# Kernel optimization log

Hardware: AMD Instinct MI355X
Metric: run time of the kernel (lower is better)

## Reference

```python
import jax, jax.numpy as jnp
import numpy as np
from jax import lax

N = 1024
N_I = 64
N_AV = 10
ALPHA = 0.5
RHO = 0.9
GAMMA = 1.0


def _make_params(seed=0):
    rng = np.random.RandomState(seed)
    diluition = 1.0 - N_AV / N
    W = rng.uniform(-1, 1, [N, N])
    W = W * (rng.uniform(0, 1, [N, N]) > diluition)
    eig = np.linalg.eigvals(W)
    W = (RHO * W / np.max(np.absolute(eig))).astype(np.float32)
    # N_i != 1 branch: gaussian input weights scaled by gamma
    W_in = (GAMMA * rng.randn(N_I, N)).astype(np.float32)
    return jnp.asarray(W), jnp.asarray(W_in)


def setup_inputs() -> dict:
    key = jax.random.key(0)
    Input = jax.random.normal(key, (128, N_I, 512), dtype=jnp.float32)
    W, W_in = _make_params()
    return {"Input": Input, "W": W, "W_in": W_in}


def reference(Input, W, W_in):
    # Input: [B, N_i, T] -> X: [B, N, T]
    B = Input.shape[0]
    x0 = jnp.zeros((B, W.shape[0]), dtype=Input.dtype)
    seq = jnp.transpose(Input, (2, 0, 1))  # [T, B, N_i]

    def step(x, s):
        x = (1.0 - ALPHA) * x + ALPHA * jnp.tanh(s @ W_in + x @ W)
        return x, x

    _, X = lax.scan(step, x0, seq)  # [T, B, N]
    return jnp.transpose(X, (1, 2, 0))  # [B, N, T]
```

## Files before the change

kernel.cpp:

```cpp
#include <hip/hip_runtime.h>
#include <hip/hip_fp16.h>
#include <cstdint>
#include <cstddef>

#define BB 128
#define NN 1024
#define NI 64
#define TT 512
#define MAXNNZ 16384
#define NE 28
#define TH 16

#define WS_OFFS   0u
#define WS_IDX    16384u
#define WS_VAL    65536u
#define WS_PERM   131072u
#define WS_IPERM  135168u
#define WS_XSTATE 139264u
#define WS_WINP   663552u
#define WS_EIDX2  925696u
#define WS_CNT16  983040u
#define WS_OFF16  1048576u
#define WS_U      1114112u

__global__ __launch_bounds__(64) void k_count16(const float* __restrict__ W, int* __restrict__ cnt16) {
    int bc = blockIdx.x;
    int s = bc & 15, g = bc >> 4;
    int col = g * 64 + threadIdx.x;
    int c = 0;
    for (int q = 0; q < 64; ++q) {
        int k = s * 64 + q;
        c += (W[(size_t)k * NN + col] != 0.0f) ? 1 : 0;
    }
    cnt16[col * 16 + s] = c;
}

__global__ __launch_bounds__(1024) void k_scan3(const int* __restrict__ cnt16, int* __restrict__ offs,
                                                int* __restrict__ off16) {
    __shared__ int s[NN];
    int tid = threadIdx.x;
    int t = 0;
#pragma unroll
    for (int q = 0; q < 16; ++q) t += cnt16[tid * 16 + q];
    s[tid] = t;
    __syncthreads();
    for (int d = 1; d < NN; d <<= 1) {
        int v = (tid >= d) ? s[tid - d] : 0;
        __syncthreads();
        s[tid] += v;
        __syncthreads();
    }
    int incl = s[tid];
    offs[tid + 1] = (incl < MAXNNZ) ? incl : MAXNNZ;
    if (tid == 0) offs[0] = 0;
    int base = incl - t;
#pragma unroll
    for (int q = 0; q < 16; ++q) {
        off16[tid * 16 + q] = base;
        base += cnt16[tid * 16 + q];
    }
}

__global__ __launch_bounds__(64) void k_fill16(const float* __restrict__ W, const int* __restrict__ off16,
                                               unsigned short* __restrict__ idx, float* __restrict__ val) {
    int bc = blockIdx.x;
    int s = bc & 15, g = bc >> 4;
    int col = g * 64 + threadIdx.x;
    int p = off16[col * 16 + s];
    for (int q = 0; q < 64; ++q) {
        int k = s * 64 + q;
        float w = W[(size_t)k * NN + col];
        if (w != 0.0f) { idx[p] = (unsigned short)k; val[p] = w; ++p; }
    }
}

__global__ __launch_bounds__(1024) void k_rankchoice(const int* __restrict__ offs,
        const unsigned short* __restrict__ gidx, int* __restrict__ perm, int* __restrict__ iperm,
        unsigned short* __restrict__ eidx2) {
    __shared__ int sc[NN];
    __shared__ unsigned short rk[NN][NE];
    __shared__ unsigned short scnt[NN];
    __shared__ unsigned short ctr[448][32];
    int n = threadIdx.x;
    sc[n] = offs[n + 1] - offs[n];
    __syncthreads();
    int myc = sc[n];
    int r = 0;
    for (int m = 0; m < NN; ++m) {
        int cm = sc[m];
        r += (cm > myc || (cm == myc && m < n)) ? 1 : 0;
    }
    perm[r] = n;
    iperm[n] = r;
    __syncthreads();
    {
        int rr = n;
        int c = perm[rr];
        int o0 = offs[c];
        int cn = offs[c + 1] - o0;
        if (cn > NE) cn = NE;
        scnt[rr] = (unsigned short)cn;
        for (int j = 0; j < cn; ++j) rk[rr][j] = (unsigned short)iperm[(int)gidx[o0 + j]];
    }
    __syncthreads();
    int tid = n;
    if (tid < 448) {
        int w = tid / NE, j = tid % NE;
        for (int b = 0; b < 32; ++b) ctr[tid][b] = 0;
        int first_addr = -1;
        for (int l = 0; l < 64; ++l) {
            int rr = 64 * w + l;
            if (j < (int)scnt[rr]) {
                int rv = (int)rk[rr][j];
                int bA = rv & 31;
                int bB = (rv ^ (rv >> 5)) & 31;
                int addr;
                if (ctr[tid][bA] <= ctr[tid][bB]) { addr = rv << 2; ctr[tid][bA]++; }
                else { addr = 4096 + (((rv & ~31) | bB) << 2); ctr[tid][bB]++; }
                eidx2[j * NN + rr] = (unsigned short)addr;
                if (first_addr < 0) first_addr = addr;
            }
        }
        unsigned short pad = (unsigned short)(first_addr < 0 ? 0 : first_addr);
        for (int l = 0; l < 64; ++l) {
            int rr = 64 * w + l;
            if (j >= (int)scnt[rr]) eidx2[j * NN + rr] = pad;
        }
    }
}

__global__ __launch_bounds__(256) void k_permwin(const float* __restrict__ Win, const int* __restrict__ perm,
                                                 float* __restrict__ Winp) {
    int idx = blockIdx.x * 256 + threadIdx.x;
    int i = idx >> 10, r = idx & 1023;
    Winp[idx] = Win[(i << 10) + perm[r]];
}

__global__ __launch_bounds__(256) void k_uproj3(const float* __restrict__ In, const float* __restrict__ Winp,
                                                __half* __restrict__ U, int t0c, int nblk) {
    int b  = blockIdx.x / nblk;
    int tq = blockIdx.x % nblk;
    int t0 = t0c + tq * 32;
    __shared__ float s[32][NI + 1];
    int tid = threadIdx.x;
    {
        int i = tid >> 2, g = tid & 3;
        const float* ip = In + ((size_t)b * NI + i) * TT + t0 + g * 8;
        float4 v0 = *(const float4*)(ip);
        float4 v1 = *(const float4*)(ip + 4);
        s[g * 8 + 0][i] = v0.x; s[g * 8 + 1][i] = v0.y;
        s[g * 8 + 2][i] = v0.z; s[g * 8 + 3][i] = v0.w;
        s[g * 8 + 4][i] = v1.x; s[g * 8 + 5][i] = v1.y;
        s[g * 8 + 6][i] = v1.z; s[g * 8 + 7][i] = v1.w;
    }
    __syncthreads();
    const float4* W4 = (const float4*)Winp;
    uint2* U2 = (uint2*)U;
    for (int th = 0; th < 2; ++th) {
        float4 acc[16];
#pragma unroll
        for (int t = 0; t < 16; ++t) acc[t] = make_float4(0.f, 0.f, 0.f, 0.f);
        for (int i = 0; i < NI; ++i) {
            float4 w = W4[(size_t)i * 256 + tid];
#pragma unroll
            for (int t = 0; t < 16; ++t) {
                float sv = s[th * 16 + t][i];
                acc[t].x = fmaf(w.x, sv, acc[t].x);
                acc[t].y = fmaf(w.y, sv, acc[t].y);
                acc[t].z = fmaf(w.z, sv, acc[t].z);
                acc[t].w = fmaf(w.w, sv, acc[t].w);
            }
        }
#pragma unroll
        for (int t = 0; t < 16; ++t) {
            __half2 h01 = __floats2half2_rn(acc[t].x, acc[t].y);
            __half2 h23 = __floats2half2_rn(acc[t].z, acc[t].w);
            uint2 pk;
            pk.x = *(unsigned int*)&h01;
            pk.y = *(unsigned int*)&h23;
            U2[((size_t)(tq * 32 + th * 16 + t) * BB + b) * 256 + tid] = pk;
        }
    }
}

__device__ __forceinline__ float fast_tanh(float z) {
    float a = fabsf(z) * 2.885390082f;
    a = fminf(a, 60.0f);
    float e = __builtin_amdgcn_exp2f(a);
    float r = 1.0f - __fdividef(2.0f, e + 1.0f);
    return z < 0.0f ? -r : r;
}

#define L28(M) \
  M(0) M(1) M(2) M(3) M(4) M(5) M(6) M(7) M(8) M(9) M(10) M(11) M(12) M(13) \
  M(14) M(15) M(16) M(17) M(18) M(19) M(20) M(21) M(22) M(23) M(24) M(25) M(26) M(27)

#define DW(i)  float w##i; int a##i;
#define IW(i)  { a##i = (int)eidx2[(i) * NN + n]; \
                 w##i = (cnt > i) ? gval[o0 + i] : 0.0f; }

#define PIN_ALL \
  asm volatile("" : "+v"(w0),"+v"(w1),"+v"(w2),"+v"(w3),"+v"(w4),"+v"(w5),"+v"(w6),"+v"(w7)); \
  asm volatile("" : "+v"(w8),"+v"(w9),"+v"(w10),"+v"(w11),"+v"(w12),"+v"(w13),"+v"(w14),"+v"(w15)); \
  asm volatile("" : "+v"(w16),"+v"(w17),"+v"(w18),"+v"(w19),"+v"(w20),"+v"(w21),"+v"(w22),"+v"(w23)); \
  asm volatile("" : "+v"(w24),"+v"(w25),"+v"(w26),"+v"(w27)); \
  asm volatile("" : "+v"(a0),"+v"(a1),"+v"(a2),"+v"(a3),"+v"(a4),"+v"(a5),"+v"(a6),"+v"(a7)); \
  asm volatile("" : "+v"(a8),"+v"(a9),"+v"(a10),"+v"(a11),"+v"(a12),"+v"(a13),"+v"(a14),"+v"(a15)); \
  asm volatile("" : "+v"(a16),"+v"(a17),"+v"(a18),"+v"(a19),"+v"(a20),"+v"(a21),"+v"(a22),"+v"(a23)); \
  asm volatile("" : "+v"(a24),"+v"(a25),"+v"(a26),"+v"(a27));

#define GRP(J, i0, i1, i2, i3) \
  if ((J) < wmax) { \
    float q0 = *(const float*)(xp + a##i0); \
    float q1 = *(const float*)(xp + a##i1); \
    float q2 = *(const float*)(xp + a##i2); \
    float q3 = *(const float*)(xp + a##i3); \
    z0 = fmaf(w##i0, q0, z0); z1 = fmaf(w##i1, q1, z1); \
    z2 = fmaf(w##i2, q2, z2); z3 = fmaf(w##i3, q3, z3); \
  }

#define GATHER_ALL \
  GRP(0, 0,1,2,3)      GRP(4, 4,5,6,7)      GRP(8, 8,9,10,11) \
  GRP(12, 12,13,14,15) GRP(16, 16,17,18,19) GRP(20, 20,21,22,23) \
  GRP(24, 24,25,26,27)

#define STEP(PH, XDST) { \
    float u = unx; \
    int tn = t + 1; tn = (tn < Tc) ? tn : (Tc - 1); \
    unx = (float)Ub[(size_t)tn * ustep]; \
    const char* xp = xb + (PH); \
    float z0 = u, z1 = 0.f, z2 = 0.f, z3 = 0.f; \
    GATHER_ALL \
    x = 0.5f * x + 0.5f * fast_tanh((z0 + z1) + (z2 + z3)); \
    XDST = x; \
    float* wb = (float*)(xb + ((PH) ^ 8192)); \
    wb[n] = x; \
    wb[NN + nB] = x; \
    __syncthreads(); \
    ++t; \
}

__global__ __launch_bounds__(1024, 4)
void k_step(const __half* __restrict__ U,
            const int* __restrict__ offs, const unsigned short* __restrict__ eidx2,
            const float* __restrict__ gval, const int* __restrict__ perm,
            float* __restrict__ out, float* __restrict__ xstate, int t0, int Tc) {
    __shared__ float xbuf[2][2][NN];
    int b = blockIdx.x, n = threadIdx.x;
    int c = perm[n];
    int nB = (n & ~31) | ((n ^ (n >> 5)) & 31);

    int o0 = offs[c];
    int cnt = offs[c + 1] - o0;
    L28(DW)
    L28(IW)
    PIN_ALL

    int wmax = cnt;
#pragma unroll
    for (int d = 1; d < 64; d <<= 1) {
        int o = __shfl_xor(wmax, d);
        wmax = wmax > o ? wmax : o;
    }
    wmax = __builtin_amdgcn_readfirstlane(wmax);

    float x = (t0 == 0) ? 0.0f : xstate[((size_t)b << 10) + n];
    xbuf[0][0][n] = x;
    xbuf[0][1][nB] = x;
    __syncthreads();

    char* xb = (char*)&xbuf[0][0][0];
    const __half* Ub = U + (size_t)b * NN + n;
    const size_t ustep = (size_t)BB * NN;
    float unx = (float)Ub[0];

    for (int tb = 0; tb < Tc; tb += TH) {
        PIN_ALL
        int t = tb;
        float y0, y1, y2, y3, y4, y5, y6, y7, y8, y9, y10, y11, y12, y13, y14, y15;
        STEP(0,    y0)
        STEP(8192, y1)
        STEP(0,    y2)
        STEP(8192, y3)
        STEP(0,    y4)
        STEP(8192, y5)
        STEP(0,    y6)
        STEP(8192, y7)
        STEP(0,    y8)
        STEP(8192, y9)
        STEP(0,    y10)
        STEP(8192, y11)
        STEP(0,    y12)
        STEP(8192, y13)
        STEP(0,    y14)
        STEP(8192, y15)
        float4* op = (float4*)(out + ((size_t)b * NN + c) * TT + (size_t)(t0 + tb));
        op[0] = make_float4(y0,  y1,  y2,  y3);
        op[1] = make_float4(y4,  y5,  y6,  y7);
        op[2] = make_float4(y8,  y9,  y10, y11);
        op[3] = make_float4(y12, y13, y14, y15);
    }
    if (Tc < TT) xstate[((size_t)b << 10) + n] = x;
}

extern "C" void kernel_launch(void* const* d_in, const int* in_sizes, int n_in,
                              void* d_out, int out_size, void* d_ws, size_t ws_size,
                              hipStream_t stream) {
    const float* In  = (const float*)d_in[0];
    const float* W   = (const float*)d_in[1];
    const float* Win = (const float*)d_in[2];
    float* out = (float*)d_out;
    char* ws = (char*)d_ws;
    int* offs           = (int*)(ws + WS_OFFS);
    unsigned short* idx = (unsigned short*)(ws + WS_IDX);
    float* val          = (float*)(ws + WS_VAL);
    int* perm           = (int*)(ws + WS_PERM);
    int* iperm          = (int*)(ws + WS_IPERM);
    float* xstate       = (float*)(ws + WS_XSTATE);
    float* Winp         = (float*)(ws + WS_WINP);
    unsigned short* eidx2 = (unsigned short*)(ws + WS_EIDX2);
    int* cnt16          = (int*)(ws + WS_CNT16);
    int* off16          = (int*)(ws + WS_OFF16);
    __half* U           = (__half*)(ws + WS_U);

    int Tc = 32;
    const int cands[5] = {512, 256, 128, 64, 32};
    for (int i = 0; i < 5; ++i) {
        if ((size_t)WS_U + (size_t)cands[i] * BB * NN * 2 <= ws_size) { Tc = cands[i]; break; }
    }

    k_count16<<<256, 64, 0, stream>>>(W, cnt16);
    k_scan3<<<1, 1024, 0, stream>>>(cnt16, offs, off16);
    k_fill16<<<256, 64, 0, stream>>>(W, off16, idx, val);
    k_rankchoice<<<1, 1024, 0, stream>>>(offs, idx, perm, iperm, eidx2);
    k_permwin<<<256, 256, 0, stream>>>(Win, perm, Winp);

    for (int t0 = 0; t0 < TT; t0 += Tc) {
        int nblk = Tc / 32;
        k_uproj3<<<BB * nblk, 256, 0, stream>>>(In, Winp, U, t0, nblk);
        k_step<<<BB, 1024, 0, stream>>>(U, offs, eidx2, val, perm, out, xstate, t0, Tc);
    }
}
```

Measured before the change: 656.2 us.

## Use fp16 dot2 for input projection and rebalance LDS bank assignment

Measured after the change: 670.3 us. 2.1% more time.

```diff
diff --git a/kernel.cpp b/kernel.cpp
--- a/kernel.cpp
+++ b/kernel.cpp
@@ -17,11 +17,25 @@
 #define WS_PERM   131072u
 #define WS_IPERM  135168u
 #define WS_XSTATE 139264u
-#define WS_WINP   663552u
+#define WS_WINPH2 663552u
 #define WS_EIDX2  925696u
 #define WS_CNT16  983040u
 #define WS_OFF16  1048576u
 #define WS_U      1114112u
+
+typedef _Float16 h2 __attribute__((ext_vector_type(2)));
+union U32H2 { unsigned u; h2 h; };
+
+__device__ __forceinline__ float fdot2f(unsigned a, unsigned b, float c) {
+#if __has_builtin(__builtin_amdgcn_fdot2)
+    U32H2 av, bv; av.u = a; bv.u = b;
+    return __builtin_amdgcn_fdot2(av.h, bv.h, c, false);
+#else
+    __half2 ah = *(__half2*)&a, bh = *(__half2*)&b;
+    return fmaf(__low2float(ah), __low2float(bh),
+                fmaf(__high2float(ah), __high2float(bh), c));
+#endif
+}
 
 __global__ __launch_bounds__(64) void k_count16(const float* __restrict__ W, int* __restrict__ cnt16) {
     int bc = blockIdx.x;
@@ -80,7 +94,7 @@
     __shared__ int sc[NN];
     __shared__ unsigned short rk[NN][NE];
     __shared__ unsigned short scnt[NN];
-    __shared__ unsigned short ctr[448][32];
+    __shared__ unsigned char ctr8[448][32];
     int n = threadIdx.x;
     sc[n] = offs[n + 1] - offs[n];
     __syncthreads();
@@ -106,17 +120,44 @@
     int tid = n;
     if (tid < 448) {
         int w = tid / NE, j = tid % NE;
-        for (int b = 0; b < 32; ++b) ctr[tid][b] = 0;
+        unsigned char* mc = &ctr8[tid][0];
+        for (int b = 0; b < 32; ++b) mc[b] = 0;
+        unsigned long long sel = 0ull;
+        for (int l = 0; l < 64; ++l) {
+            int rr = 64 * w + l;
+            if (j < (int)scnt[rr]) {
+                int rv = (int)rk[rr][j];
+                int bA = rv & 31, bB = (rv ^ (rv >> 5)) & 31;
+                if (mc[bA] <= mc[bB]) mc[bA]++;
+                else { sel |= (1ull << l); mc[bB]++; }
+            }
+        }
+        for (int sweep = 0; sweep < 16; ++sweep) {
+            bool ch = false;
+            for (int l = 0; l < 64; ++l) {
+                int rr = 64 * w + l;
+                if (j < (int)scnt[rr]) {
+                    int rv = (int)rk[rr][j];
+                    int bA = rv & 31, bB = (rv ^ (rv >> 5)) & 31;
+                    int isB = (int)((sel >> l) & 1ull);
+                    int cur = isB ? bB : bA, alt = isB ? bA : bB;
+                    if ((int)mc[cur] > (int)mc[alt] + 1) {
+                        mc[cur]--; mc[alt]++;
+                        sel ^= (1ull << l);
+                        ch = true;
+                    }
+                }
+            }
+            if (!ch) break;
+        }
         int first_addr = -1;
         for (int l = 0; l < 64; ++l) {
             int rr = 64 * w + l;
             if (j < (int)scnt[rr]) {
                 int rv = (int)rk[rr][j];
-                int bA = rv & 31;
                 int bB = (rv ^ (rv >> 5)) & 31;
-                int addr;
-                if (ctr[tid][bA] <= ctr[tid][bB]) { addr = rv << 2; ctr[tid][bA]++; }
-                else { addr = 4096 + (((rv & ~31) | bB) << 2); ctr[tid][bB]++; }
+                int addr = ((sel >> l) & 1ull) ? (4096 + (((rv & ~31) | bB) << 2))
+                                               : (rv << 2);
                 eidx2[j * NN + rr] = (unsigned short)addr;
                 if (first_addr < 0) first_addr = addr;
             }
@@ -129,46 +170,55 @@
     }
 }
 
-__global__ __launch_bounds__(256) void k_permwin(const float* __restrict__ Win, const int* __restrict__ perm,
-                                                 float* __restrict__ Winp) {
+__global__ __launch_bounds__(256) void k_permwin2(const float* __restrict__ Win, const int* __restrict__ perm,
+                                                  unsigned* __restrict__ Winph2) {
     int idx = blockIdx.x * 256 + threadIdx.x;
-    int i = idx >> 10, r = idx & 1023;
-    Winp[idx] = Win[(i << 10) + perm[r]];
-}
-
-__global__ __launch_bounds__(256) void k_uproj3(const float* __restrict__ In, const float* __restrict__ Winp,
+    int i2 = idx >> 10, r = idx & 1023;
+    int c = perm[r];
+    unsigned lo = (unsigned)__half_as_ushort(__float2half(Win[(size_t)(2 * i2) * NN + c]));
+    unsigned hi = (unsigned)__half_as_ushort(__float2half(Win[(size_t)(2 * i2 + 1) * NN + c]));
+    Winph2[idx] = lo | (hi << 16);
+}
+
+__global__ __launch_bounds__(256) void k_uproj4(const float* __restrict__ In, const unsigned* __restrict__ Winph2,
                                                 __half* __restrict__ U, int t0c, int nblk) {
     int b  = blockIdx.x / nblk;
     int tq = blockIdx.x % nblk;
     int t0 = t0c + tq * 32;
-    __shared__ float s[32][NI + 1];
+    __shared__ unsigned s2[32][33];
     int tid = threadIdx.x;
     {
         int i = tid >> 2, g = tid & 3;
         const float* ip = In + ((size_t)b * NI + i) * TT + t0 + g * 8;
         float4 v0 = *(const float4*)(ip);
         float4 v1 = *(const float4*)(ip + 4);
-        s[g * 8 + 0][i] = v0.x; s[g * 8 + 1][i] = v0.y;
-        s[g * 8 + 2][i] = v0.z; s[g * 8 + 3][i] = v0.w;
-        s[g * 8 + 4][i] = v1.x; s[g * 8 + 5][i] = v1.y;
-        s[g * 8 + 6][i] = v1.z; s[g * 8 + 7][i] = v1.w;
-    }
-    __syncthreads();
-    const float4* W4 = (const float4*)Winp;
+        __half* row = (__half*)&s2[i >> 1][0];
+        int h = i & 1;
+        row[2 * (g * 8 + 0) + h] = __float2half(v0.x);
+        row[2 * (g * 8 + 1) + h] = __float2half(v0.y);
+        row[2 * (g * 8 + 2) + h] = __float2half(v0.z);
+        row[2 * (g * 8 + 3) + h] = __float2half(v0.w);
+        row[2 * (g * 8 + 4) + h] = __float2half(v1.x);
+        row[2 * (g * 8 + 5) + h] = __float2half(v1.y);
+        row[2 * (g * 8 + 6) + h] = __float2half(v1.z);
+        row[2 * (g * 8 + 7) + h] = __float2half(v1.w);
+    }
+    __syncthreads();
+    const uint4* W4 = (const uint4*)Winph2;
     uint2* U2 = (uint2*)U;
     for (int th = 0; th < 2; ++th) {
         float4 acc[16];
 #pragma unroll
         for (int t = 0; t < 16; ++t) acc[t] = make_float4(0.f, 0.f, 0.f, 0.f);
-        for (int i = 0; i < NI; ++i) {
-            float4 w = W4[(size_t)i * 256 + tid];
+        for (int i2 = 0; i2 < 32; ++i2) {
+            uint4 w = W4[(size_t)i2 * 256 + tid];
 #pragma unroll
             for (int t = 0; t < 16; ++t) {
-                float sv = s[th * 16 + t][i];
-                acc[t].x = fmaf(w.x, sv, acc[t].x);
-                acc[t].y = fmaf(w.y, sv, acc[t].y);
-                acc[t].z = fmaf(w.z, sv, acc[t].z);
-                acc[t].w = fmaf(w.w, sv, acc[t].w);
+                unsigned sv = s2[i2][th * 16 + t];
+                acc[t].x = fdot2f(w.x, sv, acc[t].x);
+                acc[t].y = fdot2f(w.y, sv, acc[t].y);
+                acc[t].z = fdot2f(w.z, sv, acc[t].z);
+                acc[t].w = fdot2f(w.w, sv, acc[t].w);
             }
         }
 #pragma unroll
@@ -317,7 +367,7 @@
     int* perm           = (int*)(ws + WS_PERM);
     int* iperm          = (int*)(ws + WS_IPERM);
     float* xstate       = (float*)(ws + WS_XSTATE);
-    float* Winp         = (float*)(ws + WS_WINP);
+    unsigned* Winph2    = (unsigned*)(ws + WS_WINPH2);
     unsigned short* eidx2 = (unsigned short*)(ws + WS_EIDX2);
     int* cnt16          = (int*)(ws + WS_CNT16);
     int* off16          = (int*)(ws + WS_OFF16);
@@ -333,11 +383,11 @@
     k_scan3<<<1, 1024, 0, stream>>>(cnt16, offs, off16);
     k_fill16<<<256, 64, 0, stream>>>(W, off16, idx, val);
     k_rankchoice<<<1, 1024, 0, stream>>>(offs, idx, perm, iperm, eidx2);
-    k_permwin<<<256, 256, 0, stream>>>(Win, perm, Winp);
+    k_permwin2<<<128, 256, 0, stream>>>(Win, perm, Winph2);
 
     for (int t0 = 0; t0 < TT; t0 += Tc) {
         int nblk = Tc / 32;
-        k_uproj3<<<BB * nblk, 256, 0, stream>>>(In, Winp, U, t0, nblk);
+        k_uproj4<<<BB * nblk, 256, 0, stream>>>(In, Winph2, U, t0, nblk);
         k_step<<<BB, 1024, 0, stream>>>(U, offs, eidx2, val, perm, out, xstate, t0, Tc);
     }
 }
```
